# Kernel tuning notes

Measured on AMD Instinct MI355X. Metric: run time of the kernel, lower is better.

Reference implementation:

```python
import jax, jax.numpy as jnp
import numpy as np

N, D_IN, D_OUT, E = 100000, 64, 64, 800000
C_IN, C_OUT = 1.0, 1.0
MAX_NORM = 1e6   # manifold.max_norm clamp used by PseudoHypAgg
EPS = 1e-15
BALL_EPS = 4e-3  # Poincare-ball projection margin (fp32)


def _artanh(x):
    return jnp.arctanh(jnp.clip(x, -1 + 1e-7, 1 - 1e-7))


def _proj(x, c):
    # project onto the open Poincare ball of curvature c
    sqrt_c = jnp.sqrt(c)
    norm = jnp.clip(jnp.linalg.norm(x, axis=-1, keepdims=True), EPS)
    maxn = (1.0 - BALL_EPS) / sqrt_c
    return jnp.where(norm > maxn, x / norm * maxn, x)


def _expmap0(u, c):
    sqrt_c = jnp.sqrt(c)
    n = jnp.clip(jnp.linalg.norm(u, axis=-1, keepdims=True), EPS)
    return jnp.tanh(sqrt_c * n) * u / (sqrt_c * n)


def _logmap0(p, c):
    sqrt_c = jnp.sqrt(c)
    n = jnp.clip(jnp.linalg.norm(p, axis=-1, keepdims=True), EPS)
    return _artanh(sqrt_c * n) * p / (sqrt_c * n)


def _mobius_add(x, y, c):
    x2 = jnp.sum(x * x, -1, keepdims=True)
    y2 = jnp.sum(y * y, -1, keepdims=True)
    xy = jnp.sum(x * y, -1, keepdims=True)
    num = (1 + 2 * c * xy + c * y2) * x + (1 - c * x2) * y
    den = 1 + 2 * c * xy + c * c * x2 * y2
    return num / jnp.clip(den, EPS)


def _mobius_matvec(M, x, c):
    sqrt_c = jnp.sqrt(c)
    x_norm = jnp.clip(jnp.linalg.norm(x, axis=-1, keepdims=True), EPS)
    mx = x @ M.T  # [N, D_OUT]
    mx_norm = jnp.clip(jnp.linalg.norm(mx, axis=-1, keepdims=True), EPS)
    res = jnp.tanh(mx_norm / x_norm * _artanh(sqrt_c * x_norm)) * mx / (mx_norm * sqrt_c)
    zero = jnp.all(mx == 0, axis=-1, keepdims=True)
    return jnp.where(zero, jnp.zeros_like(res), res)


def setup_inputs() -> dict:
    key = jax.random.key(0)
    k1, k2, k3, k4, k5, k6 = jax.random.split(key, 6)
    # node features: small-norm points inside the unit ball
    x = _proj(0.05 * jax.random.normal(k1, (N, D_IN), jnp.float32), C_IN)
    W = jax.random.normal(k2, (D_OUT, D_IN), jnp.float32) / np.float32(np.sqrt(D_IN))
    b = 0.01 * jax.random.normal(k3, (D_OUT,), jnp.float32)
    edge_row = jax.random.randint(k4, (E,), 0, N, jnp.int32)
    edge_col = jax.random.randint(k5, (E,), 0, N, jnp.int32)
    edge_val = jax.random.uniform(k6, (E,), jnp.float32) / 16.0  # ~normalized adj weights
    return {"x": x, "W": W, "b": b, "edge_row": edge_row,
            "edge_col": edge_col, "edge_val": edge_val}


def reference(x, W, b, edge_row, edge_col, edge_val):
    # --- PseudoHypLinear (eval mode: dropout inactive) ---
    mv = _mobius_matvec(W, x, C_IN)
    res = _proj(mv, C_IN)
    hyp_b = _proj(_expmap0(b[None, :], C_IN), C_IN)  # proj_tan0 is identity on the ball
    h = _proj(_mobius_add(res, hyp_b, C_IN), C_IN)
    # --- PseudoHypAgg (use_att=False): spmm in tangent space at origin ---
    x_t = _logmap0(h, C_IN)                              # [N, D_OUT]
    msg = edge_val[:, None] * x_t[edge_col]              # [E, D_OUT]
    support_t = jax.ops.segment_sum(msg, edge_row, num_segments=N)
    support_t = jnp.minimum(support_t, MAX_NORM)         # clamp(max=manifold.max_norm)
    h = _proj(_expmap0(support_t, C_IN), C_IN)           # proj_tan0 identity
    # --- PseudoHypAct: act in tangent at origin (c_in), re-embed with c_out ---
    xt = jax.nn.relu(_logmap0(h, C_IN))
    return _proj(_expmap0(xt, C_OUT), C_OUT)
```

## Files before the change

kernel.cpp:

```cpp
#include <hip/hip_runtime.h>
#include <hip/hip_fp16.h>
#include <math.h>

#define DD 64
#define BK 128
#define BCAP 2048
#define NBKT_MAX 800
#define CHUNK 8192
constexpr float FEPS = 1e-15f;
constexpr float MAXN = 1.0f - 4e-3f;

__device__ __forceinline__ float wsum(float v) {
    v += __shfl_xor(v, 32);
    v += __shfl_xor(v, 16);
    v += __shfl_xor(v, 8);
    v += __shfl_xor(v, 4);
    v += __shfl_xor(v, 2);
    v += __shfl_xor(v, 1);
    return v;
}

__device__ __forceinline__ int wave_incl_scan(int v) {
    int lane = threadIdx.x & 63;
    #pragma unroll
    for (int d = 1; d < 64; d <<= 1) {
        int t = __shfl_up(v, d);
        if (lane >= d) v += t;
    }
    return v;
}

__device__ __forceinline__ float artanh_c(float x) {
    x = fminf(fmaxf(x, -1.f + 1e-7f), 1.f - 1e-7f);
    return 0.5f * logf((1.f + x) / (1.f - x));
}

struct SmemLin {
    float tile[DD * 65];
    float red0[8][DD];
    float red1[8][DD];
    float hb[66];
    float Ab[DD], Bb[DD];
};
struct SmemBin {
    int lcnt[NBKT_MAX];
    int goff[NBKT_MAX];
};

__global__ __launch_bounds__(512) void kfused(
    const float* __restrict__ x, const float* __restrict__ W,
    const float* __restrict__ bvec, __half* __restrict__ xth,
    const int* __restrict__ erow, const int* __restrict__ ecol,
    const float* __restrict__ eval_, int* __restrict__ gcnt,
    int2* __restrict__ binned, int nbkt, int n_edges, int n_nodes, int nbB) {
    __shared__ union { SmemLin lin; SmemBin bin; } sm;
    const int t = threadIdx.x;

    if ((int)blockIdx.x < nbB) {
        const int eb = blockIdx.x * CHUNK;
        for (int i = t; i < nbkt; i += 512) sm.bin.lcnt[i] = 0;
        __syncthreads();
        int rk[16];
        #pragma unroll
        for (int i = 0; i < 16; ++i) {
            int e = eb + i * 512 + t;
            rk[i] = -1;
            if (e < n_edges) {
                int r = erow[e];
                int bkt = r >> 7;
                int rank = atomicAdd(&sm.bin.lcnt[bkt], 1);
                rk[i] = (bkt << 20) | ((r & (BK - 1)) << 13) | rank;
            }
        }
        __syncthreads();
        for (int i = t; i < nbkt; i += 512) {
            int c = sm.bin.lcnt[i];
            if (c > 0) sm.bin.goff[i] = atomicAdd(&gcnt[i], c);
        }
        __syncthreads();
        #pragma unroll
        for (int i = 0; i < 16; ++i) {
            int e = eb + i * 512 + t;
            if (e >= n_edges) continue;
            int bkt = rk[i] >> 20, lr = (rk[i] >> 13) & 127, rank = rk[i] & 8191;
            int pos = sm.bin.goff[bkt] + rank;
            if (pos < BCAP)
                binned[(size_t)bkt * BCAP + pos] =
                    make_int2((lr << 17) | ecol[e], __float_as_int(eval_[e]));
        }
        return;
    }

    const int lane = t & 63;
    const int w = t >> 6;
    const int n0 = ((int)blockIdx.x - nbB) * DD;

    #pragma unroll
    for (int rep = 0; rep < 2; ++rep) {
        int i = rep * 512 + t;
        int nd = i >> 4, q = i & 15;
        int node = n0 + nd;
        const float4* src = reinterpret_cast<const float4*>(
            x + (size_t)(node < n_nodes ? node : 0) * DD);
        float4 v = src[q];
        float* d = &sm.lin.tile[nd * 65 + q * 4];
        d[0] = v.x; d[1] = v.y; d[2] = v.z; d[3] = v.w;
    }
    if (t < 64) {
        float bv = bvec[t];
        float n2 = wsum(bv * bv);
        float n = fmaxf(sqrtf(n2), FEPS);
        float th = tanhf(n);
        float p = th * (bv / n);
        float pn = th * (sqrtf(n2) / n);
        float pn_c = fmaxf(pn, FEPS);
        if (pn_c > MAXN) p *= MAXN / pn_c;
        sm.lin.hb[t] = p;
        float p2 = wsum(p * p);
        if (t == 0) sm.lin.hb[DD] = p2;
    }
    __syncthreads();

    const int jbase = __builtin_amdgcn_readfirstlane(w) * 8;
    float mx[8] = {0.f, 0.f, 0.f, 0.f, 0.f, 0.f, 0.f, 0.f};
    float xn2 = 0.f;
    #pragma unroll
    for (int kk = 0; kk < 4; ++kk) {
        float xv[16];
        #pragma unroll
        for (int ki = 0; ki < 16; ++ki)
            xv[ki] = sm.lin.tile[lane * 65 + kk * 16 + ki];
        #pragma unroll
        for (int ki = 0; ki < 16; ++ki)
            xn2 = fmaf(xv[ki], xv[ki], xn2);
        #pragma unroll
        for (int jj = 0; jj < 8; ++jj) {
            const float* Wr = W + (jbase + jj) * DD + kk * 16;
            float a = mx[jj];
            #pragma unroll
            for (int ki = 0; ki < 16; ++ki) a = fmaf(Wr[ki], xv[ki], a);
            mx[jj] = a;
        }
    }
    float mx2p = 0.f, mxhp = 0.f;
    #pragma unroll
    for (int jj = 0; jj < 8; ++jj) {
        mx2p = fmaf(mx[jj], mx[jj], mx2p);
        mxhp = fmaf(mx[jj], sm.lin.hb[jbase + jj], mxhp);
    }
    sm.lin.red0[w][lane] = mx2p;
    sm.lin.red1[w][lane] = mxhp;
    __syncthreads();

    if (t < 64) {
        float mx2 = 0.f, mxh = 0.f;
        #pragma unroll
        for (int ww = 0; ww < 8; ++ww) {
            mx2 += sm.lin.red0[ww][t];
            mxh += sm.lin.red1[ww][t];
        }
        float xn = fmaxf(sqrtf(xn2), FEPS);
        float mxn = fmaxf(sqrtf(mx2), FEPS);
        float th = tanhf((mxn / xn) * artanh_c(xn));
        float sres = (mx2 == 0.f) ? 0.f : th / mxn;
        float rn = (mx2 == 0.f) ? 0.f : th * (sqrtf(mx2) / mxn);
        float rn_c = fmaxf(rn, FEPS);
        float s1 = (rn_c > MAXN) ? sres * (MAXN / rn_c) : sres;
        float x2r = s1 * s1 * mx2;
        float xy = s1 * mxh;
        float y2 = sm.lin.hb[DD];
        float ca = 1.f + 2.f * xy + y2;
        float cb = 1.f - x2r;
        float rden = 1.f / fmaxf(1.f + 2.f * xy + x2r * y2, FEPS);
        float al = ca * s1 * rden;
        float be = cb * rden;
        float h2 = al * al * mx2 + 2.f * al * be * mxh + be * be * y2;
        float hn = fmaxf(sqrtf(h2), FEPS);
        float sh = 1.f;
        if (hn > MAXN) { sh = MAXN / hn; hn = MAXN; }
        float su = sh * (artanh_c(hn) / hn);
        sm.lin.Ab[t] = su * al;
        sm.lin.Bb[t] = su * be;
    }
    __syncthreads();

    int node = n0 + lane;
    if (node < n_nodes) {
        float A = sm.lin.Ab[lane], B = sm.lin.Bb[lane];
        float u[8];
        #pragma unroll
        for (int jj = 0; jj < 8; ++jj)
            u[jj] = fmaf(A, mx[jj], B * sm.lin.hb[jbase + jj]);
        __half2 p0 = __floats2half2_rn(u[0], u[1]);
        __half2 p1 = __floats2half2_rn(u[2], u[3]);
        __half2 p2 = __floats2half2_rn(u[4], u[5]);
        __half2 p3 = __floats2half2_rn(u[6], u[7]);
        uint4 o;
        o.x = *reinterpret_cast<unsigned int*>(&p0);
        o.y = *reinterpret_cast<unsigned int*>(&p1);
        o.z = *reinterpret_cast<unsigned int*>(&p2);
        o.w = *reinterpret_cast<unsigned int*>(&p3);
        *reinterpret_cast<uint4*>(xth + (size_t)node * DD + jbase) = o;
    }
}

__device__ __forceinline__ void agg_epilogue(
    float4 acc, int row, int fl, float* __restrict__ out) {
    float4 s;
    s.x = fminf(acc.x, 1e6f); s.y = fminf(acc.y, 1e6f);
    s.z = fminf(acc.z, 1e6f); s.w = fminf(acc.w, 1e6f);
    float4 rs;
    rs.x = fmaxf(s.x, 0.f); rs.y = fmaxf(s.y, 0.f);
    rs.z = fmaxf(s.z, 0.f); rs.w = fmaxf(s.w, 0.f);
    float n2p = s.x * s.x + s.y * s.y + s.z * s.z + s.w * s.w;
    float sp2p = rs.x * rs.x + rs.y * rs.y + rs.z * rs.z + rs.w * rs.w;
    #pragma unroll
    for (int m = 1; m < 16; m <<= 1) {
        n2p += __shfl_xor(n2p, m);
        sp2p += __shfl_xor(sp2p, m);
    }
    float n = fmaxf(sqrtf(n2p), FEPS);
    float th = tanhf(n);
    float c1 = th / n;
    float pn = th * (sqrtf(n2p) / n);
    float pn_c = fmaxf(pn, FEPS);
    if (pn_c > MAXN) { c1 *= MAXN / pn_c; pn_c = MAXN; }
    float k1 = (artanh_c(pn_c) / pn_c) * c1;
    float u2 = k1 * k1 * sp2p;
    float un = fmaxf(sqrtf(u2), FEPS);
    float t2 = tanhf(un);
    float k2 = (t2 / un) * k1;
    float on = t2 * (sqrtf(u2) / un);
    float on_c = fmaxf(on, FEPS);
    if (on_c > MAXN) k2 *= MAXN / on_c;
    float4 o;
    o.x = k2 * rs.x; o.y = k2 * rs.y; o.z = k2 * rs.z; o.w = k2 * rs.w;
    reinterpret_cast<float4*>(out)[(size_t)row * 16 + fl] = o;
}

__global__ __launch_bounds__(512) void kagg2(
    const int* __restrict__ gcnt, const int2* __restrict__ binned,
    const __half* __restrict__ xth, float* __restrict__ out, int n_nodes) {
    __shared__ int hist[BK], offs[BK], cur[BK];
    __shared__ int2 srt[BCAP];
    const int t = threadIdx.x;
    const int b = blockIdx.x;
    for (int i = t; i < BK; i += 512) hist[i] = 0;
    __syncthreads();
    const int nrec = min(gcnt[b], BCAP);
    const int2* rec = binned + (size_t)b * BCAP;
    int2 rc[BCAP / 512];
    #pragma unroll
    for (int i = 0; i < BCAP / 512; ++i) {
        int j = i * 512 + t;
        if (j < nrec) {
            rc[i] = rec[j];
            atomicAdd(&hist[rc[i].x >> 17], 1);
        }
    }
    __syncthreads();
    if (t < 64) {
        int v = hist[t];
        int s = wave_incl_scan(v);
        offs[t] = s - v;
    }
    __syncthreads();
    if (t < 64) {
        int c = offs[63] + hist[63];
        int v = hist[64 + t];
        int s = wave_incl_scan(v);
        offs[64 + t] = c + s - v;
    }
    __syncthreads();
    for (int i = t; i < BK; i += 512) cur[i] = offs[i];
    __syncthreads();
    #pragma unroll
    for (int i = 0; i < BCAP / 512; ++i) {
        int j = i * 512 + t;
        if (j < nrec) {
            int lr = rc[i].x >> 17;
            int p = atomicAdd(&cur[lr], 1);
            srt[p] = make_int2(rc[i].x & 0x1FFFF, rc[i].y);
        }
    }
    __syncthreads();

    const int g = t >> 4, fl = t & 15;
    #pragma unroll
    for (int it = 0; it < BK / 32; ++it) {
        int lr = it * 32 + g;
        int row = b * BK + lr;
        if (row >= n_nodes) continue;
        int beg = offs[lr], end = beg + hist[lr];
        float4 acc = make_float4(0.f, 0.f, 0.f, 0.f);
        int j = beg;
        for (; j + 7 < end; j += 8) {
            int2 e[8];
            float2 r[8];
            #pragma unroll
            for (int q = 0; q < 8; ++q) e[q] = srt[j + q];
            #pragma unroll
            for (int q = 0; q < 8; ++q)
                r[q] = *reinterpret_cast<const float2*>(
                    xth + (size_t)e[q].x * DD + fl * 4);
            #pragma unroll
            for (int q = 0; q < 8; ++q) {
                float wq = __int_as_float(e[q].y);
                float2 lo = __half22float2(*reinterpret_cast<__half2*>(&r[q].x));
                float2 hi = __half22float2(*reinterpret_cast<__half2*>(&r[q].y));
                acc.x = fmaf(wq, lo.x, acc.x); acc.y = fmaf(wq, lo.y, acc.y);
                acc.z = fmaf(wq, hi.x, acc.z); acc.w = fmaf(wq, hi.y, acc.w);
            }
        }
        for (; j + 3 < end; j += 4) {
            int2 e[4];
            float2 r[4];
            #pragma unroll
            for (int q = 0; q < 4; ++q) e[q] = srt[j + q];
            #pragma unroll
            for (int q = 0; q < 4; ++q)
                r[q] = *reinterpret_cast<const float2*>(
                    xth + (size_t)e[q].x * DD + fl * 4);
            #pragma unroll
            for (int q = 0; q < 4; ++q) {
                float wq = __int_as_float(e[q].y);
                float2 lo = __half22float2(*reinterpret_cast<__half2*>(&r[q].x));
                float2 hi = __half22float2(*reinterpret_cast<__half2*>(&r[q].y));
                acc.x = fmaf(wq, lo.x, acc.x); acc.y = fmaf(wq, lo.y, acc.y);
                acc.z = fmaf(wq, hi.x, acc.z); acc.w = fmaf(wq, hi.y, acc.w);
            }
        }
        for (; j < end; ++j) {
            int2 e = srt[j];
            float2 r0 = *reinterpret_cast<const float2*>(
                xth + (size_t)e.x * DD + fl * 4);
            float w0 = __int_as_float(e.y);
            float2 lo = __half22float2(*reinterpret_cast<__half2*>(&r0.x));
            float2 hi = __half22float2(*reinterpret_cast<__half2*>(&r0.y));
            acc.x = fmaf(w0, lo.x, acc.x); acc.y = fmaf(w0, lo.y, acc.y);
            acc.z = fmaf(w0, hi.x, acc.z); acc.w = fmaf(w0, hi.y, acc.w);
        }
        agg_epilogue(acc, row, fl, out);
    }
}

extern "C" void kernel_launch(void* const* d_in, const int* in_sizes, int n_in,
                              void* d_out, int out_size, void* d_ws, size_t ws_size,
                              hipStream_t stream) {
    const float* x     = (const float*)d_in[0];
    const float* W     = (const float*)d_in[1];
    const float* b     = (const float*)d_in[2];
    const int*   erow  = (const int*)d_in[3];
    const int*   ecol  = (const int*)d_in[4];
    const float* eval_ = (const float*)d_in[5];
    const int n_nodes = in_sizes[0] / DD;
    const int n_edges = in_sizes[3];
    float* out = (float*)d_out;

    const int NBKT = (n_nodes + BK - 1) / BK;

    int2*   binned = (int2*)d_ws;
    __half* xth    = (__half*)(binned + (size_t)NBKT * BCAP);
    int*    gcnt   = (int*)(xth + (size_t)n_nodes * DD);

    const int nbB = (n_edges + CHUNK - 1) / CHUNK;
    const int nbL = (n_nodes + DD - 1) / DD;

    hipMemsetAsync(gcnt, 0, NBKT_MAX * sizeof(int), stream);
    kfused<<<nbB + nbL, 512, 0, stream>>>(x, W, b, xth, erow, ecol, eval_,
                                          gcnt, binned, NBKT, n_edges, n_nodes, nbB);
    kagg2<<<NBKT, 512, 0, stream>>>(gcnt, binned, xth, out, n_nodes);
}
```

Measured before the change: 136.3 us.

## Compute hyperbolic linear matvec with fp16 MFMA per wave, drop shared-memory staging

Replaces the scalar FMA matvec, which staged x in LDS and reduced across waves, with per-wave 16x16x32 fp16 MFMA tiles. Each wave handles 16 nodes and does its norm reductions with shuffles, so the shared tile and block barriers go away. Linear blocks now cover 128 nodes each. This cuts FMA work and LDS traffic, but x and W are rounded to fp16 before the multiply, which adds precision error, and output stores become scalar half writes.

```diff
diff --git a/kernel.cpp b/kernel.cpp
--- a/kernel.cpp
+++ b/kernel.cpp
@@ -9,6 +9,9 @@
 #define CHUNK 8192
 constexpr float FEPS = 1e-15f;
 constexpr float MAXN = 1.0f - 4e-3f;
+
+typedef _Float16 f16x8 __attribute__((ext_vector_type(8)));
+typedef float f32x4 __attribute__((ext_vector_type(4)));
 
 __device__ __forceinline__ float wsum(float v) {
     v += __shfl_xor(v, 32);
@@ -35,30 +38,19 @@
     return 0.5f * logf((1.f + x) / (1.f - x));
 }
 
-struct SmemLin {
-    float tile[DD * 65];
-    float red0[8][DD];
-    float red1[8][DD];
-    float hb[66];
-    float Ab[DD], Bb[DD];
-};
-struct SmemBin {
-    int lcnt[NBKT_MAX];
-    int goff[NBKT_MAX];
-};
-
 __global__ __launch_bounds__(512) void kfused(
     const float* __restrict__ x, const float* __restrict__ W,
     const float* __restrict__ bvec, __half* __restrict__ xth,
     const int* __restrict__ erow, const int* __restrict__ ecol,
     const float* __restrict__ eval_, int* __restrict__ gcnt,
     int2* __restrict__ binned, int nbkt, int n_edges, int n_nodes, int nbB) {
-    __shared__ union { SmemLin lin; SmemBin bin; } sm;
     const int t = threadIdx.x;
 
     if ((int)blockIdx.x < nbB) {
+        __shared__ int lcnt[NBKT_MAX];
+        __shared__ int goff[NBKT_MAX];
         const int eb = blockIdx.x * CHUNK;
-        for (int i = t; i < nbkt; i += 512) sm.bin.lcnt[i] = 0;
+        for (int i = t; i < nbkt; i += 512) lcnt[i] = 0;
         __syncthreads();
         int rk[16];
         #pragma unroll
@@ -68,14 +60,14 @@
             if (e < n_edges) {
                 int r = erow[e];
                 int bkt = r >> 7;
-                int rank = atomicAdd(&sm.bin.lcnt[bkt], 1);
+                int rank = atomicAdd(&lcnt[bkt], 1);
                 rk[i] = (bkt << 20) | ((r & (BK - 1)) << 13) | rank;
             }
         }
         __syncthreads();
         for (int i = t; i < nbkt; i += 512) {
-            int c = sm.bin.lcnt[i];
-            if (c > 0) sm.bin.goff[i] = atomicAdd(&gcnt[i], c);
+            int c = lcnt[i];
+            if (c > 0) goff[i] = atomicAdd(&gcnt[i], c);
         }
         __syncthreads();
         #pragma unroll
@@ -83,7 +75,7 @@
             int e = eb + i * 512 + t;
             if (e >= n_edges) continue;
             int bkt = rk[i] >> 20, lr = (rk[i] >> 13) & 127, rank = rk[i] & 8191;
-            int pos = sm.bin.goff[bkt] + rank;
+            int pos = goff[bkt] + rank;
             if (pos < BCAP)
                 binned[(size_t)bkt * BCAP + pos] =
                     make_int2((lr << 17) | ecol[e], __float_as_int(eval_[e]));
@@ -92,74 +84,98 @@
     }
 
     const int lane = t & 63;
-    const int w = t >> 6;
-    const int n0 = ((int)blockIdx.x - nbB) * DD;
-
-    #pragma unroll
-    for (int rep = 0; rep < 2; ++rep) {
-        int i = rep * 512 + t;
-        int nd = i >> 4, q = i & 15;
-        int node = n0 + nd;
-        const float4* src = reinterpret_cast<const float4*>(
-            x + (size_t)(node < n_nodes ? node : 0) * DD);
-        float4 v = src[q];
-        float* d = &sm.lin.tile[nd * 65 + q * 4];
-        d[0] = v.x; d[1] = v.y; d[2] = v.z; d[3] = v.w;
-    }
-    if (t < 64) {
-        float bv = bvec[t];
-        float n2 = wsum(bv * bv);
-        float n = fmaxf(sqrtf(n2), FEPS);
-        float th = tanhf(n);
-        float p = th * (bv / n);
-        float pn = th * (sqrtf(n2) / n);
-        float pn_c = fmaxf(pn, FEPS);
-        if (pn_c > MAXN) p *= MAXN / pn_c;
-        sm.lin.hb[t] = p;
-        float p2 = wsum(p * p);
-        if (t == 0) sm.lin.hb[DD] = p2;
-    }
-    __syncthreads();
-
-    const int jbase = __builtin_amdgcn_readfirstlane(w) * 8;
-    float mx[8] = {0.f, 0.f, 0.f, 0.f, 0.f, 0.f, 0.f, 0.f};
-    float xn2 = 0.f;
-    #pragma unroll
-    for (int kk = 0; kk < 4; ++kk) {
-        float xv[16];
-        #pragma unroll
-        for (int ki = 0; ki < 16; ++ki)
-            xv[ki] = sm.lin.tile[lane * 65 + kk * 16 + ki];
-        #pragma unroll
-        for (int ki = 0; ki < 16; ++ki)
-            xn2 = fmaf(xv[ki], xv[ki], xn2);
-        #pragma unroll
-        for (int jj = 0; jj < 8; ++jj) {
-            const float* Wr = W + (jbase + jj) * DD + kk * 16;
-            float a = mx[jj];
-            #pragma unroll
-            for (int ki = 0; ki < 16; ++ki) a = fmaf(Wr[ki], xv[ki], a);
-            mx[jj] = a;
-        }
-    }
-    float mx2p = 0.f, mxhp = 0.f;
-    #pragma unroll
-    for (int jj = 0; jj < 8; ++jj) {
-        mx2p = fmaf(mx[jj], mx[jj], mx2p);
-        mxhp = fmaf(mx[jj], sm.lin.hb[jbase + jj], mxhp);
-    }
-    sm.lin.red0[w][lane] = mx2p;
-    sm.lin.red1[w][lane] = mxhp;
-    __syncthreads();
-
-    if (t < 64) {
-        float mx2 = 0.f, mxh = 0.f;
-        #pragma unroll
-        for (int ww = 0; ww < 8; ++ww) {
-            mx2 += sm.lin.red0[ww][t];
-            mxh += sm.lin.red1[ww][t];
-        }
-        float xn = fmaxf(sqrtf(xn2), FEPS);
+    const int wv = t >> 6;
+    const int nw = ((int)blockIdx.x - nbB) * 128 + wv * 16;
+    if (nw >= n_nodes) return;
+    const int r16 = lane & 15;
+    const int khi = lane >> 4;
+
+    float bv = bvec[lane];
+    float bn2 = wsum(bv * bv);
+    float bn = fmaxf(sqrtf(bn2), FEPS);
+    float bth = tanhf(bn);
+    float p = bth * (bv / bn);
+    float pnrm = bth * (sqrtf(bn2) / bn);
+    float pn_c = fmaxf(pnrm, FEPS);
+    if (pn_c > MAXN) p *= MAXN / pn_c;
+    float y2 = wsum(p * p);
+    float hbj[4];
+    #pragma unroll
+    for (int jt = 0; jt < 4; ++jt)
+        hbj[jt] = __shfl(p, jt * 16 + r16);
+
+    int nodeA = nw + r16;
+    int nca = (nodeA < n_nodes) ? nodeA : (n_nodes - 1);
+    const float* xrow = x + (size_t)nca * DD + khi * 8;
+    f16x8 a[2];
+    float xpart = 0.f;
+    #pragma unroll
+    for (int kc = 0; kc < 2; ++kc) {
+        float4 v0 = *reinterpret_cast<const float4*>(xrow + kc * 32);
+        float4 v1 = *reinterpret_cast<const float4*>(xrow + kc * 32 + 4);
+        xpart += v0.x * v0.x + v0.y * v0.y + v0.z * v0.z + v0.w * v0.w
+               + v1.x * v1.x + v1.y * v1.y + v1.z * v1.z + v1.w * v1.w;
+        a[kc][0] = (_Float16)v0.x; a[kc][1] = (_Float16)v0.y;
+        a[kc][2] = (_Float16)v0.z; a[kc][3] = (_Float16)v0.w;
+        a[kc][4] = (_Float16)v1.x; a[kc][5] = (_Float16)v1.y;
+        a[kc][6] = (_Float16)v1.z; a[kc][7] = (_Float16)v1.w;
+    }
+    xpart += __shfl_xor(xpart, 16);
+    xpart += __shfl_xor(xpart, 32);
+    float xn2d[4];
+    #pragma unroll
+    for (int r = 0; r < 4; ++r)
+        xn2d[r] = __shfl(xpart, khi * 4 + r);
+
+    f16x8 bfr[4][2];
+    #pragma unroll
+    for (int jt = 0; jt < 4; ++jt) {
+        const float* wrow = W + (size_t)(jt * 16 + r16) * DD + khi * 8;
+        #pragma unroll
+        for (int kc = 0; kc < 2; ++kc) {
+            float4 v0 = *reinterpret_cast<const float4*>(wrow + kc * 32);
+            float4 v1 = *reinterpret_cast<const float4*>(wrow + kc * 32 + 4);
+            bfr[jt][kc][0] = (_Float16)v0.x; bfr[jt][kc][1] = (_Float16)v0.y;
+            bfr[jt][kc][2] = (_Float16)v0.z; bfr[jt][kc][3] = (_Float16)v0.w;
+            bfr[jt][kc][4] = (_Float16)v1.x; bfr[jt][kc][5] = (_Float16)v1.y;
+            bfr[jt][kc][6] = (_Float16)v1.z; bfr[jt][kc][7] = (_Float16)v1.w;
+        }
+    }
+
+    f32x4 d[4];
+    #pragma unroll
+    for (int jt = 0; jt < 4; ++jt) {
+        d[jt] = (f32x4){0.f, 0.f, 0.f, 0.f};
+        #pragma unroll
+        for (int kc = 0; kc < 2; ++kc)
+            d[jt] = __builtin_amdgcn_mfma_f32_16x16x32_f16(a[kc], bfr[jt][kc], d[jt], 0, 0, 0);
+    }
+
+    float mx2p[4], mxhp[4];
+    #pragma unroll
+    for (int r = 0; r < 4; ++r) {
+        float s2 = 0.f, sh = 0.f;
+        #pragma unroll
+        for (int jt = 0; jt < 4; ++jt) {
+            s2 = fmaf(d[jt][r], d[jt][r], s2);
+            sh = fmaf(d[jt][r], hbj[jt], sh);
+        }
+        mx2p[r] = s2; mxhp[r] = sh;
+    }
+    #pragma unroll
+    for (int m = 1; m < 16; m <<= 1) {
+        #pragma unroll
+        for (int r = 0; r < 4; ++r) {
+            mx2p[r] += __shfl_xor(mx2p[r], m);
+            mxhp[r] += __shfl_xor(mxhp[r], m);
+        }
+    }
+
+    float As[4], Bs[4];
+    #pragma unroll
+    for (int r = 0; r < 4; ++r) {
+        float mx2 = mx2p[r], mxh = mxhp[r];
+        float xn = fmaxf(sqrtf(xn2d[r]), FEPS);
         float mxn = fmaxf(sqrtf(mx2), FEPS);
         float th = tanhf((mxn / xn) * artanh_c(xn));
         float sres = (mx2 == 0.f) ? 0.f : th / mxn;
@@ -168,7 +184,6 @@
         float s1 = (rn_c > MAXN) ? sres * (MAXN / rn_c) : sres;
         float x2r = s1 * s1 * mx2;
         float xy = s1 * mxh;
-        float y2 = sm.lin.hb[DD];
         float ca = 1.f + 2.f * xy + y2;
         float cb = 1.f - x2r;
         float rden = 1.f / fmaxf(1.f + 2.f * xy + x2r * y2, FEPS);
@@ -179,28 +194,19 @@
         float sh = 1.f;
         if (hn > MAXN) { sh = MAXN / hn; hn = MAXN; }
         float su = sh * (artanh_c(hn) / hn);
-        sm.lin.Ab[t] = su * al;
-        sm.lin.Bb[t] = su * be;
-    }
-    __syncthreads();
-
-    int node = n0 + lane;
-    if (node < n_nodes) {
-        float A = sm.lin.Ab[lane], B = sm.lin.Bb[lane];
-        float u[8];
-        #pragma unroll
-        for (int jj = 0; jj < 8; ++jj)
-            u[jj] = fmaf(A, mx[jj], B * sm.lin.hb[jbase + jj]);
-        __half2 p0 = __floats2half2_rn(u[0], u[1]);
-        __half2 p1 = __floats2half2_rn(u[2], u[3]);
-        __half2 p2 = __floats2half2_rn(u[4], u[5]);
-        __half2 p3 = __floats2half2_rn(u[6], u[7]);
-        uint4 o;
-        o.x = *reinterpret_cast<unsigned int*>(&p0);
-        o.y = *reinterpret_cast<unsigned int*>(&p1);
-        o.z = *reinterpret_cast<unsigned int*>(&p2);
-        o.w = *reinterpret_cast<unsigned int*>(&p3);
-        *reinterpret_cast<uint4*>(xth + (size_t)node * DD + jbase) = o;
+        As[r] = su * al;
+        Bs[r] = su * be;
+    }
+
+    #pragma unroll
+    for (int r = 0; r < 4; ++r) {
+        int node = nw + khi * 4 + r;
+        if (node >= n_nodes) continue;
+        #pragma unroll
+        for (int jt = 0; jt < 4; ++jt) {
+            float u = fmaf(As[r], d[jt][r], Bs[r] * hbj[jt]);
+            xth[(size_t)node * DD + jt * 16 + r16] = __float2half_rn(u);
+        }
     }
 }
 
@@ -364,7 +370,7 @@
     int*    gcnt   = (int*)(xth + (size_t)n_nodes * DD);
 
     const int nbB = (n_edges + CHUNK - 1) / CHUNK;
-    const int nbL = (n_nodes + DD - 1) / DD;
+    const int nbL = (n_nodes + 127) / 128;
 
     hipMemsetAsync(gcnt, 0, NBKT_MAX * sizeof(int), stream);
     kfused<<<nbB + nbL, 512, 0, stream>>>(x, W, b, xth, erow, ecol, eval_,
```

Result: slower. 145.7 us (+6.9%).
